# Kernel tuning notes

Measured on AMD Instinct MI355X. Metric: run time of the kernel, lower is better.

Reference implementation:

```python
import jax, jax.numpy as jnp
import numpy as np

E = 512      # embedding_size
H = 8        # heads
FF = 4 * E   # ffn hidden
EPS = 1e-5


def layer_norm(x, gamma, beta):
    mu = jnp.mean(x, axis=-1, keepdims=True)
    var = jnp.mean((x - mu) ** 2, axis=-1, keepdims=True)
    return (x - mu) * jax.lax.rsqrt(var + EPS) * gamma + beta


def setup_inputs() -> dict:
    key = jax.random.key(0)
    ks = jax.random.split(key, 12)
    N, L = 4, 2048
    s = E ** -0.5
    return {
        "x": jax.random.normal(ks[0], (N, L, E), jnp.float32),
        "wq": jax.random.normal(ks[1], (E, E), jnp.float32) * s,
        "wk": jax.random.normal(ks[2], (E, E), jnp.float32) * s,
        "wv": jax.random.normal(ks[3], (E, E), jnp.float32) * s,
        "wo": jax.random.normal(ks[4], (E, E), jnp.float32) * s,
        "bo": jnp.zeros((E,), jnp.float32),
        "g1": jnp.ones((E,), jnp.float32),
        "b1": jnp.zeros((E,), jnp.float32),
        "g2": jnp.ones((E,), jnp.float32),
        "b2": jnp.zeros((E,), jnp.float32),
        "w1": jax.random.normal(ks[5], (E, FF), jnp.float32) * s,
        "bf1": jnp.zeros((FF,), jnp.float32),
        "w2": jax.random.normal(ks[6], (FF, E), jnp.float32) * (FF ** -0.5),
        "bf2": jnp.zeros((E,), jnp.float32),
    }


def reference(x, wq, wk, wv, wo, bo, g1, b1, g2, b2, w1, bf1, w2, bf2):
    N, L, _ = x.shape
    skip = x
    h = layer_norm(x, g1, b1)
    # attention (weights stored as [in, out])
    q = (h @ wq).reshape(N, L, H, E // H)
    k = (h @ wk).reshape(N, L, H, E // H)
    v = (h @ wv).reshape(N, L, H, E // H)
    # NOTE: source scales by embedding_size**-0.5 (not head_dim)
    scores = jnp.einsum('nqhd,nkhd->nhqk', q, k) * (E ** -0.5)
    attn = jax.nn.softmax(scores, axis=-1)
    out = jnp.einsum('nhql,nlhd->nqhd', attn, v).reshape(N, L, E)
    x = out @ wo + bo + skip
    skip = x
    h = layer_norm(x, g2, b2)  # dropout is identity in eval
    h = jax.nn.silu(h @ w1 + bf1) @ w2 + bf2
    return h + skip
```

## Files before the change

kernel.cpp:

```cpp
#include <hip/hip_runtime.h>
#include <hip/hip_bf16.h>

typedef __bf16 bf16;
typedef __attribute__((ext_vector_type(2))) __bf16 bf16x2;
typedef __attribute__((ext_vector_type(8))) __bf16 bf16x8;
typedef __attribute__((ext_vector_type(4))) float f32x4;
typedef __attribute__((ext_vector_type(16))) float f32x16;

#define MFMA16(a, b, c) __builtin_amdgcn_mfma_f32_16x16x32_bf16((a), (b), (c), 0, 0, 0)
#define MFMA32(a, b, c) __builtin_amdgcn_mfma_f32_32x32x16_bf16((a), (b), (c), 0, 0, 0)


__device__ __forceinline__ void load_lds16(const bf16* g, bf16* l) {
    __builtin_amdgcn_global_load_lds(
        (const __attribute__((address_space(1))) void*)g,
        (__attribute__((address_space(3))) void*)l, 16, 0, 0);
}

__device__ __forceinline__ float fexp2(float x) { return __builtin_amdgcn_exp2f(x); }

__global__ void cvt_all(const float* __restrict__ wq, const float* __restrict__ wk,
                        const float* __restrict__ wv, const float* __restrict__ wo,
                        const float* __restrict__ w1, const float* __restrict__ w2,
                        bf16* __restrict__ wqkv_t, bf16* __restrict__ wo_t,
                        bf16* __restrict__ w1_t, bf16* __restrict__ w2_t) {
    __shared__ float t[64][65];
    const int b = blockIdx.x;
    const float* src; bf16* dst;
    int sstride, dstride, r0, c0, dr0;
    if (b < 192) {
        int bx = b % 24, by = b / 24;
        int j0 = bx * 64;
        src = (j0 < 512) ? wq : (j0 < 1024) ? wk : wv;
        sstride = 512; r0 = by * 64; c0 = j0 & 511;
        dst = wqkv_t; dstride = 512; dr0 = j0;
    } else if (b < 256) {
        int tt = b - 192; int bx = tt % 8, by = tt / 8;
        src = wo; sstride = 512; r0 = by * 64; c0 = bx * 64;
        dst = wo_t; dstride = 512; dr0 = c0;
    } else if (b < 512) {
        int tt = b - 256; int bx = tt % 32, by = tt / 32;
        src = w1; sstride = 2048; r0 = by * 64; c0 = bx * 64;
        dst = w1_t; dstride = 512; dr0 = c0;
    } else {
        int tt = b - 512; int bx = tt % 8, by = tt / 8;
        src = w2; sstride = 512; r0 = by * 64; c0 = bx * 64;
        dst = w2_t; dstride = 2048; dr0 = c0;
    }
    #pragma unroll
    for (int p = 0; p < 16; p++) {
        int lin = threadIdx.x + p * 256;
        int rr = lin >> 6, cc = lin & 63;
        t[rr][cc] = src[(size_t)(r0 + rr) * sstride + c0 + cc];
    }
    __syncthreads();
    #pragma unroll
    for (int p = 0; p < 16; p++) {
        int lin = threadIdx.x + p * 256;
        int cc = lin >> 6, rr = lin & 63;
        dst[(size_t)(dr0 + cc) * dstride + r0 + rr] = (bf16)t[rr][cc];
    }
}

__global__ void ln_kernel(const float* __restrict__ x, const float* __restrict__ g,
                          const float* __restrict__ b, bf16* __restrict__ out) {
    int row = blockIdx.x * 4 + (threadIdx.x >> 6);
    int lane = threadIdx.x & 63;
    const float4* xr = (const float4*)(x + (size_t)row * 512);
    float4 v0 = xr[lane];
    float4 v1 = xr[lane + 64];
    float s  = v0.x + v0.y + v0.z + v0.w + v1.x + v1.y + v1.z + v1.w;
    float sq = v0.x*v0.x + v0.y*v0.y + v0.z*v0.z + v0.w*v0.w
             + v1.x*v1.x + v1.y*v1.y + v1.z*v1.z + v1.w*v1.w;
    #pragma unroll
    for (int d = 1; d < 64; d <<= 1) { s += __shfl_xor(s, d); sq += __shfl_xor(sq, d); }
    float mean = s * (1.f / 512.f);
    float var  = sq * (1.f / 512.f) - mean * mean;
    float rs   = rsqrtf(var + 1e-5f);
    const float4* gv = (const float4*)g;
    const float4* bv = (const float4*)b;
    float4 ga = gv[lane], gb = gv[lane + 64];
    float4 ba = bv[lane], bb = bv[lane + 64];
    bf16* orow = out + (size_t)row * 512;
    int c0 = lane * 4;
    orow[c0 + 0]   = (bf16)((v0.x - mean) * rs * ga.x + ba.x);
    orow[c0 + 1]   = (bf16)((v0.y - mean) * rs * ga.y + ba.y);
    orow[c0 + 2]   = (bf16)((v0.z - mean) * rs * ga.z + ba.z);
    orow[c0 + 3]   = (bf16)((v0.w - mean) * rs * ga.w + ba.w);
    orow[c0 + 256] = (bf16)((v1.x - mean) * rs * gb.x + bb.x);
    orow[c0 + 257] = (bf16)((v1.y - mean) * rs * gb.y + bb.y);
    orow[c0 + 258] = (bf16)((v1.z - mean) * rs * gb.z + bb.z);
    orow[c0 + 259] = (bf16)((v1.w - mean) * rs * gb.w + bb.w);
}

template<int KD, int ND, int EPI>
__global__ __launch_bounds__(256, 3) void gemm_k(
        const bf16* __restrict__ A, const bf16* __restrict__ Bt,
        const float* __restrict__ bias, void* __restrict__ outp) {
    __shared__ bf16 As[128 * 64];
    __shared__ bf16 Bs[128 * 64];
    const int bm = blockIdx.x, bn = blockIdx.y;
    const int tid = threadIdx.x;
    const int w = tid >> 6, lane = tid & 63;
    const int wm = (w >> 1) * 64, wn = (w & 1) * 64;
    const int lr = lane & 15, lq = lane >> 4, lr7 = lane & 7;
    const int srow = lane >> 3, gslot = lane & 7;
    f32x4 acc[4][4] = {};
    const bf16* Ab = A + (size_t)bm * 128 * KD;
    const bf16* Bb = Bt + (size_t)bn * 128 * KD;
    const int gcol = (gslot ^ srow) * 8;
    for (int k0 = 0; k0 < KD; k0 += 64) {
        __syncthreads();
        #pragma unroll
        for (int s = 0; s < 4; s++) {
            int rbase = w * 32 + s * 8;
            int row = rbase + srow;
            load_lds16(&Ab[(size_t)row * KD + k0 + gcol], &As[rbase * 64]);
            load_lds16(&Bb[(size_t)row * KD + k0 + gcol], &Bs[rbase * 64]);
        }
        __syncthreads();
        #pragma unroll
        for (int ks = 0; ks < 2; ks++) {
            bf16x8 af[4], bfr[4];
            #pragma unroll
            for (int mi = 0; mi < 4; mi++) {
                int row = wm + mi * 16 + lr;
                af[mi] = *(const bf16x8*)&As[row * 64 + (((ks * 4 + lq) ^ lr7) << 3)];
            }
            #pragma unroll
            for (int ni = 0; ni < 4; ni++) {
                int row = wn + ni * 16 + lr;
                bfr[ni] = *(const bf16x8*)&Bs[row * 64 + (((ks * 4 + lq) ^ lr7) << 3)];
            }
            #pragma unroll
            for (int mi = 0; mi < 4; mi++)
                #pragma unroll
                for (int ni = 0; ni < 4; ni++)
                    acc[mi][ni] = MFMA16(af[mi], bfr[ni], acc[mi][ni]);
        }
    }
    #pragma unroll
    for (int mi = 0; mi < 4; mi++)
        #pragma unroll
        for (int ni = 0; ni < 4; ni++)
            #pragma unroll
            for (int r = 0; r < 4; r++) {
                int row = bm * 128 + wm + mi * 16 + lq * 4 + r;
                int col = bn * 128 + wn + ni * 16 + lr;
                float v = acc[mi][ni][r];
                size_t off = (size_t)row * ND + col;
                if constexpr (EPI == 0) {
                    ((bf16*)outp)[off] = (bf16)v;
                } else {
                    v += bias[col];
                    v = v / (1.f + __expf(-v));
                    ((bf16*)outp)[off] = (bf16)v;
                }
            }
}

template<int KD>
__global__ __launch_bounds__(256, 4) void gemm64(
        const bf16* __restrict__ A, const bf16* __restrict__ Bt,
        const float* __restrict__ bias, const float* __restrict__ resid,
        float* __restrict__ outp) {
    __shared__ bf16 As[64 * 64];
    __shared__ bf16 Bs[64 * 64];
    const int bm = blockIdx.x, bn = blockIdx.y;
    const int tid = threadIdx.x;
    const int w = tid >> 6, lane = tid & 63;
    const int wm = (w >> 1) * 32, wn = (w & 1) * 32;
    const int lr = lane & 15, lq = lane >> 4, lr7 = lane & 7;
    const int srow = lane >> 3, gslot = lane & 7;
    f32x4 acc[2][2] = {};
    const bf16* Ab = A + (size_t)bm * 64 * KD;
    const bf16* Bb = Bt + (size_t)bn * 64 * KD;
    const int gcol = (gslot ^ srow) * 8;
    for (int k0 = 0; k0 < KD; k0 += 64) {
        __syncthreads();
        #pragma unroll
        for (int s = 0; s < 2; s++) {
            int rbase = w * 16 + s * 8;
            int row = rbase + srow;
            load_lds16(&Ab[(size_t)row * KD + k0 + gcol], &As[rbase * 64]);
            load_lds16(&Bb[(size_t)row * KD + k0 + gcol], &Bs[rbase * 64]);
        }
        __syncthreads();
        #pragma unroll
        for (int ks = 0; ks < 2; ks++) {
            bf16x8 af[2], bfr[2];
            #pragma unroll
            for (int mi = 0; mi < 2; mi++) {
                int row = wm + mi * 16 + lr;
                af[mi] = *(const bf16x8*)&As[row * 64 + (((ks * 4 + lq) ^ lr7) << 3)];
            }
            #pragma unroll
            for (int ni = 0; ni < 2; ni++) {
                int row = wn + ni * 16 + lr;
                bfr[ni] = *(const bf16x8*)&Bs[row * 64 + (((ks * 4 + lq) ^ lr7) << 3)];
            }
            #pragma unroll
            for (int mi = 0; mi < 2; mi++)
                #pragma unroll
                for (int ni = 0; ni < 2; ni++)
                    acc[mi][ni] = MFMA16(af[mi], bfr[ni], acc[mi][ni]);
        }
    }
    #pragma unroll
    for (int mi = 0; mi < 2; mi++)
        #pragma unroll
        for (int ni = 0; ni < 2; ni++)
            #pragma unroll
            for (int r = 0; r < 4; r++) {
                int row = bm * 64 + wm + mi * 16 + lq * 4 + r;
                int col = bn * 64 + wn + ni * 16 + lr;
                size_t off = (size_t)row * 512 + col;
                outp[off] = acc[mi][ni][r] + bias[col] + resid[off];
            }
}

__global__ void pack_kv(const bf16* __restrict__ qkvb, bf16* __restrict__ Kfrag,
                        bf16* __restrict__ Vfrag) {
    __shared__ bf16 t[64 * 72];
    const int nh = blockIdx.x & 31, lt = blockIdx.x >> 5;
    const int n = nh >> 3, h = nh & 7;
    const int tid = threadIdx.x;
    #pragma unroll
    for (int p = 0; p < 2; p++) {
        int cid = tid + p * 256;
        int key = lt * 64 + (cid >> 3);
        int dc = cid & 7;
        bf16x8 kv = *(const bf16x8*)&qkvb[(size_t)(n * 2048 + key) * 1536
                                          + 512 + h * 64 + dc * 8];
        int kb = key >> 5, l5 = key & 31;
        int c = dc >> 1, g = dc & 1;
        *(bf16x8*)&Kfrag[(size_t)(((nh * 64 + kb) * 4 + c) * 64 + g * 32 + l5) * 8] = kv;
    }
    #pragma unroll
    for (int p = 0; p < 2; p++) {
        int lin = tid + p * 256;
        int rr = lin >> 3, cc = lin & 7;
        bf16x8 v = *(const bf16x8*)&qkvb[(size_t)(n * 2048 + lt * 64 + rr) * 1536
                                         + 1024 + h * 64 + cc * 8];
        *(bf16x8*)&t[rr * 72 + (cc ^ (rr & 7)) * 8] = v;
    }
    __syncthreads();
    #pragma unroll
    for (int p = 0; p < 2; p++) {
        int lin = tid + p * 256;
        int dd = lin & 63, llc = lin >> 6 | (p << 2);
        bf16x8 o;
        #pragma unroll
        for (int j = 0; j < 8; j++) {
            int ll = llc * 8 + j;
            o[j] = t[ll * 72 + (((dd >> 3) ^ (ll & 7)) * 8) + (dd & 7)];
        }
        int token0 = lt * 64 + llc * 8;
        int kb = token0 >> 5;
        int tl5 = token0 & 31;
        int r = ((tl5 >> 4) << 1) | (dd >> 5);
        int lane = ((token0 >> 3) & 1) * 32 + (dd & 31);
        *(bf16x8*)&Vfrag[(size_t)(((nh * 64 + kb) * 4 + r) * 64 + lane) * 8] = o;
    }
}

__global__ __launch_bounds__(512, 4) void attn_kernel(const bf16* __restrict__ qkv,
                                                      const bf16* __restrict__ Kfrag,
                                                      const bf16* __restrict__ Vfrag,
                                                      bf16* __restrict__ aout) {
    __shared__ float accbuf[4][32][64];
    __shared__ float psumbuf[4][32];
    __shared__ bf16 Ot[4][32 * 72];
    const int b = blockIdx.x;
    const int nh = b & 31;
    const int qt = b >> 5;
    const int n = nh >> 3, h = nh & 7;
    const int tid = threadIdx.x, w = tid >> 6, lane = tid & 63;
    const int qsub = w & 3, ks = w >> 2;
    const int lq5 = lane & 31, g = lane >> 5;
    const float cf = 0.04419417382415922f * 1.4426950408889634f;

    const bf16* Qp = qkv + (size_t)(n * 2048 + qt * 128 + qsub * 32 + lq5) * 1536
                     + h * 64 + g * 8;
    bf16x8 qf[4];
    #pragma unroll
    for (int c = 0; c < 4; c++) {
        bf16x8 raw = *(const bf16x8*)(Qp + c * 16);
        #pragma unroll
        for (int j = 0; j < 8; j++) qf[c][j] = (bf16)((float)raw[j] * cf);
    }

    f32x16 acc0 = {0}, acc1 = {0};
    float psum = 0.f;

    const bf16* Kb = Kfrag + (size_t)((nh * 64 + ks * 32) * 4) * 512 + lane * 8;
    const bf16* Vb = Vfrag + (size_t)((nh * 64 + ks * 32) * 4) * 512 + lane * 8;

    bf16x8 kfn[4];
    kfn[0] = *(const bf16x8*)(Kb);
    kfn[1] = *(const bf16x8*)(Kb + 512);
    kfn[2] = *(const bf16x8*)(Kb + 1024);
    kfn[3] = *(const bf16x8*)(Kb + 1536);

    #pragma unroll 2
    for (int t = 0; t < 32; t++) {
        const bf16* Vc = Vb + t * 2048;
        bf16x8 v00 = *(const bf16x8*)(Vc);
        bf16x8 v01 = *(const bf16x8*)(Vc + 512);
        bf16x8 v10 = *(const bf16x8*)(Vc + 1024);
        bf16x8 v11 = *(const bf16x8*)(Vc + 1536);

        f32x16 st = {0};
        st = MFMA32(kfn[0], qf[0], st);
        st = MFMA32(kfn[1], qf[1], st);
        st = MFMA32(kfn[2], qf[2], st);
        st = MFMA32(kfn[3], qf[3], st);

        if (t < 31) {
            const bf16* Kt = Kb + (t + 1) * 2048;
            kfn[0] = *(const bf16x8*)(Kt);
            kfn[1] = *(const bf16x8*)(Kt + 512);
            kfn[2] = *(const bf16x8*)(Kt + 1024);
            kfn[3] = *(const bf16x8*)(Kt + 1536);
        }

        #pragma unroll
        for (int h16 = 0; h16 < 2; h16++) {
            uint32_t pk[4];
            #pragma unroll
            for (int i = 0; i < 4; i++) {
                float p0 = fexp2(fminf(st[8 * h16 + 2 * i], 60.f));
                float p1 = fexp2(fminf(st[8 * h16 + 2 * i + 1], 60.f));
                psum += p0 + p1;
                union { uint32_t u; bf16x2 hh; } cvu;
                cvu.hh = bf16x2{(bf16)p0, (bf16)p1};
                pk[i] = cvu.u;
            }
            uint32_t s0 = g ? pk[0] : pk[2];
            uint32_t s1 = g ? pk[1] : pk[3];
            uint32_t r0 = (uint32_t)__shfl_xor((int)s0, 32);
            uint32_t r1 = (uint32_t)__shfl_xor((int)s1, 32);
            union { uint4 u; bf16x8 v; } pf;
            pf.u = g == 0 ? uint4{pk[0], pk[1], r0, r1}
                          : uint4{r0, r1, pk[2], pk[3]};
            if (h16 == 0) {
                acc0 = MFMA32(v00, pf.v, acc0);
                acc1 = MFMA32(v01, pf.v, acc1);
            } else {
                acc0 = MFMA32(v10, pf.v, acc0);
                acc1 = MFMA32(v11, pf.v, acc1);
            }
        }
    }

    float tot = psum + __shfl_xor(psum, 32);

    if (ks == 1) {
        #pragma unroll
        for (int r = 0; r < 16; r++) {
            accbuf[qsub][r][lane]      = acc0[r];
            accbuf[qsub][16 + r][lane] = acc1[r];
        }
        if (g == 0) psumbuf[qsub][lq5] = tot;
    }
    __syncthreads();
    if (ks == 0) {
        float inv = 1.f / (tot + psumbuf[qsub][lq5]);
        bf16* ot = Ot[qsub];
        #pragma unroll
        for (int r = 0; r < 16; r++) {
            float a0 = acc0[r] + accbuf[qsub][r][lane];
            float a1 = acc1[r] + accbuf[qsub][16 + r][lane];
            int d0 = (r & 3) + 8 * (r >> 2) + 4 * g;
            ot[lq5 * 72 + d0]      = (bf16)(a0 * inv);
            ot[lq5 * 72 + d0 + 32] = (bf16)(a1 * inv);
        }
        __builtin_amdgcn_s_waitcnt(0);
        #pragma unroll
        for (int i = 0; i < 4; i++) {
            int tq = i * 8 + (lane >> 3);
            bf16x8 ov = *(const bf16x8*)&ot[tq * 72 + (lane & 7) * 8];
            *(bf16x8*)&aout[(size_t)(n * 2048 + qt * 128 + qsub * 32 + tq) * 512
                            + h * 64 + (lane & 7) * 8] = ov;
        }
    }
}

extern "C" void kernel_launch(void* const* d_in, const int* in_sizes, int n_in,
                              void* d_out, int out_size, void* d_ws, size_t ws_size,
                              hipStream_t stream) {
    (void)in_sizes; (void)n_in; (void)out_size; (void)ws_size;
    const float* x   = (const float*)d_in[0];
    const float* wq  = (const float*)d_in[1];
    const float* wk  = (const float*)d_in[2];
    const float* wv  = (const float*)d_in[3];
    const float* wo  = (const float*)d_in[4];
    const float* bo  = (const float*)d_in[5];
    const float* g1  = (const float*)d_in[6];
    const float* b1  = (const float*)d_in[7];
    const float* g2  = (const float*)d_in[8];
    const float* b2  = (const float*)d_in[9];
    const float* w1  = (const float*)d_in[10];
    const float* bf1 = (const float*)d_in[11];
    const float* w2  = (const float*)d_in[12];
    const float* bf2 = (const float*)d_in[13];
    float* out = (float*)d_out;

    char* p = (char*)d_ws;
    bf16*  h1     = (bf16*)p;  p += (size_t)8192 * 512 * 2;
    bf16*  qkvb   = (bf16*)p;  p += (size_t)8192 * 1536 * 2;
    bf16*  aout   = (bf16*)p;  p += (size_t)8192 * 512 * 2;
    float* x2     = (float*)p; p += (size_t)8192 * 512 * 4;
    bf16*  ff1    = (bf16*)p;  p += (size_t)8192 * 2048 * 2;
    bf16*  wqkv_t = (bf16*)p;  p += (size_t)1536 * 512 * 2;
    bf16*  wo_t   = (bf16*)p;  p += (size_t)512 * 512 * 2;
    bf16*  w1_t   = (bf16*)p;  p += (size_t)2048 * 512 * 2;
    bf16*  w2_t   = (bf16*)p;  p += (size_t)512 * 2048 * 2;
    bf16*  Kfrag  = (bf16*)ff1;
    bf16*  Vfrag  = Kfrag + (size_t)8192 * 512;

    cvt_all<<<768, 256, 0, stream>>>(wq, wk, wv, wo, w1, w2, wqkv_t, wo_t, w1_t, w2_t);

    ln_kernel<<<2048, 256, 0, stream>>>(x, g1, b1, h1);
    gemm_k<512, 1536, 0><<<dim3(64, 12), 256, 0, stream>>>(h1, wqkv_t, nullptr, qkvb);
    pack_kv<<<1024, 256, 0, stream>>>(qkvb, Kfrag, Vfrag);
    attn_kernel<<<512, 512, 0, stream>>>(qkvb, Kfrag, Vfrag, aout);
    gemm64<512><<<dim3(128, 8), 256, 0, stream>>>(aout, wo_t, bo, x, x2);
    ln_kernel<<<2048, 256, 0, stream>>>(x2, g2, b2, h1);
    gemm_k<512, 2048, 2><<<dim3(64, 16), 256, 0, stream>>>(h1, w1_t, bf1, ff1);
    gemm64<2048><<<dim3(128, 8), 256, 0, stream>>>(ff1, w2_t, bf2, x2, out);
}
```

Measured before the change: 243.7 us.

## Fuse LN1 into weight conversion, scatter K/V in QKV epilogue, retile output GEMMs

Merges the first layernorm into the weight-conversion launch and drops the separate pack_kv kernel by having the QKV GEMM scatter K and V directly into fragment layouts while writing Q to a compact buffer. The 64x64 gemm64 kernels for the Wo and W2 projections are replaced with the 128x128 gemm_k using a new residual-add epilogue. The clamp before exp2 in attention is also removed. These cut launches and a round trip through qkvb, at the cost of scattered 2-byte stores in the QKV epilogue and only 256 blocks for the N=512 GEMMs. Removing the clamp risks overflow if scores are large.

```diff
diff --git a/kernel.cpp b/kernel.cpp
--- a/kernel.cpp
+++ b/kernel.cpp
@@ -19,13 +19,45 @@
 
 __device__ __forceinline__ float fexp2(float x) { return __builtin_amdgcn_exp2f(x); }
 
-__global__ void cvt_all(const float* __restrict__ wq, const float* __restrict__ wk,
-                        const float* __restrict__ wv, const float* __restrict__ wo,
-                        const float* __restrict__ w1, const float* __restrict__ w2,
-                        bf16* __restrict__ wqkv_t, bf16* __restrict__ wo_t,
-                        bf16* __restrict__ w1_t, bf16* __restrict__ w2_t) {
+__global__ void front_kernel(const float* __restrict__ x, const float* __restrict__ g1,
+                             const float* __restrict__ b1, bf16* __restrict__ h1,
+                             const float* __restrict__ wq, const float* __restrict__ wk,
+                             const float* __restrict__ wv, const float* __restrict__ wo,
+                             const float* __restrict__ w1, const float* __restrict__ w2,
+                             bf16* __restrict__ wqkv_t, bf16* __restrict__ wo_t,
+                             bf16* __restrict__ w1_t, bf16* __restrict__ w2_t) {
     __shared__ float t[64][65];
-    const int b = blockIdx.x;
+    if (blockIdx.x < 2048) {
+        int row = blockIdx.x * 4 + (threadIdx.x >> 6);
+        int lane = threadIdx.x & 63;
+        const float4* xr = (const float4*)(x + (size_t)row * 512);
+        float4 v0 = xr[lane];
+        float4 v1 = xr[lane + 64];
+        float s  = v0.x + v0.y + v0.z + v0.w + v1.x + v1.y + v1.z + v1.w;
+        float sq = v0.x*v0.x + v0.y*v0.y + v0.z*v0.z + v0.w*v0.w
+                 + v1.x*v1.x + v1.y*v1.y + v1.z*v1.z + v1.w*v1.w;
+        #pragma unroll
+        for (int d = 1; d < 64; d <<= 1) { s += __shfl_xor(s, d); sq += __shfl_xor(sq, d); }
+        float mean = s * (1.f / 512.f);
+        float var  = sq * (1.f / 512.f) - mean * mean;
+        float rs   = rsqrtf(var + 1e-5f);
+        const float4* gv = (const float4*)g1;
+        const float4* bv = (const float4*)b1;
+        float4 ga = gv[lane], gb = gv[lane + 64];
+        float4 ba = bv[lane], bb = bv[lane + 64];
+        bf16* orow = h1 + (size_t)row * 512;
+        int c0 = lane * 4;
+        orow[c0 + 0]   = (bf16)((v0.x - mean) * rs * ga.x + ba.x);
+        orow[c0 + 1]   = (bf16)((v0.y - mean) * rs * ga.y + ba.y);
+        orow[c0 + 2]   = (bf16)((v0.z - mean) * rs * ga.z + ba.z);
+        orow[c0 + 3]   = (bf16)((v0.w - mean) * rs * ga.w + ba.w);
+        orow[c0 + 256] = (bf16)((v1.x - mean) * rs * gb.x + bb.x);
+        orow[c0 + 257] = (bf16)((v1.y - mean) * rs * gb.y + bb.y);
+        orow[c0 + 258] = (bf16)((v1.z - mean) * rs * gb.z + bb.z);
+        orow[c0 + 259] = (bf16)((v1.w - mean) * rs * gb.w + bb.w);
+        return;
+    }
+    const int b = blockIdx.x - 2048;
     const float* src; bf16* dst;
     int sstride, dstride, r0, c0, dr0;
     if (b < 192) {
@@ -96,7 +128,8 @@
 template<int KD, int ND, int EPI>
 __global__ __launch_bounds__(256, 3) void gemm_k(
         const bf16* __restrict__ A, const bf16* __restrict__ Bt,
-        const float* __restrict__ bias, void* __restrict__ outp) {
+        const float* __restrict__ bias, const float* __restrict__ resid,
+        void* __restrict__ outp) {
     __shared__ bf16 As[128 * 64];
     __shared__ bf16 Bs[128 * 64];
     const int bm = blockIdx.x, bn = blockIdx.y;
@@ -151,6 +184,8 @@
                 size_t off = (size_t)row * ND + col;
                 if constexpr (EPI == 0) {
                     ((bf16*)outp)[off] = (bf16)v;
+                } else if constexpr (EPI == 1) {
+                    ((float*)outp)[off] = v + bias[col] + resid[off];
                 } else {
                     v += bias[col];
                     v = v / (1.f + __expf(-v));
@@ -159,112 +194,80 @@
             }
 }
 
-template<int KD>
-__global__ __launch_bounds__(256, 4) void gemm64(
+__global__ __launch_bounds__(256, 3) void gemm_qkv(
         const bf16* __restrict__ A, const bf16* __restrict__ Bt,
-        const float* __restrict__ bias, const float* __restrict__ resid,
-        float* __restrict__ outp) {
-    __shared__ bf16 As[64 * 64];
-    __shared__ bf16 Bs[64 * 64];
+        bf16* __restrict__ Qb, bf16* __restrict__ Kfrag, bf16* __restrict__ Vfrag) {
+    __shared__ bf16 As[128 * 64];
+    __shared__ bf16 Bs[128 * 64];
     const int bm = blockIdx.x, bn = blockIdx.y;
     const int tid = threadIdx.x;
     const int w = tid >> 6, lane = tid & 63;
-    const int wm = (w >> 1) * 32, wn = (w & 1) * 32;
+    const int wm = (w >> 1) * 64, wn = (w & 1) * 64;
     const int lr = lane & 15, lq = lane >> 4, lr7 = lane & 7;
     const int srow = lane >> 3, gslot = lane & 7;
-    f32x4 acc[2][2] = {};
-    const bf16* Ab = A + (size_t)bm * 64 * KD;
-    const bf16* Bb = Bt + (size_t)bn * 64 * KD;
+    f32x4 acc[4][4] = {};
+    const bf16* Ab = A + (size_t)bm * 128 * 512;
+    const bf16* Bb = Bt + (size_t)bn * 128 * 512;
     const int gcol = (gslot ^ srow) * 8;
-    for (int k0 = 0; k0 < KD; k0 += 64) {
+    for (int k0 = 0; k0 < 512; k0 += 64) {
         __syncthreads();
         #pragma unroll
-        for (int s = 0; s < 2; s++) {
-            int rbase = w * 16 + s * 8;
+        for (int s = 0; s < 4; s++) {
+            int rbase = w * 32 + s * 8;
             int row = rbase + srow;
-            load_lds16(&Ab[(size_t)row * KD + k0 + gcol], &As[rbase * 64]);
-            load_lds16(&Bb[(size_t)row * KD + k0 + gcol], &Bs[rbase * 64]);
+            load_lds16(&Ab[(size_t)row * 512 + k0 + gcol], &As[rbase * 64]);
+            load_lds16(&Bb[(size_t)row * 512 + k0 + gcol], &Bs[rbase * 64]);
         }
         __syncthreads();
         #pragma unroll
         for (int ks = 0; ks < 2; ks++) {
-            bf16x8 af[2], bfr[2];
-            #pragma unroll
-            for (int mi = 0; mi < 2; mi++) {
+            bf16x8 af[4], bfr[4];
+            #pragma unroll
+            for (int mi = 0; mi < 4; mi++) {
                 int row = wm + mi * 16 + lr;
                 af[mi] = *(const bf16x8*)&As[row * 64 + (((ks * 4 + lq) ^ lr7) << 3)];
             }
             #pragma unroll
-            for (int ni = 0; ni < 2; ni++) {
+            for (int ni = 0; ni < 4; ni++) {
                 int row = wn + ni * 16 + lr;
                 bfr[ni] = *(const bf16x8*)&Bs[row * 64 + (((ks * 4 + lq) ^ lr7) << 3)];
             }
             #pragma unroll
-            for (int mi = 0; mi < 2; mi++)
+            for (int mi = 0; mi < 4; mi++)
                 #pragma unroll
-                for (int ni = 0; ni < 2; ni++)
+                for (int ni = 0; ni < 4; ni++)
                     acc[mi][ni] = MFMA16(af[mi], bfr[ni], acc[mi][ni]);
         }
     }
     #pragma unroll
-    for (int mi = 0; mi < 2; mi++)
-        #pragma unroll
-        for (int ni = 0; ni < 2; ni++)
+    for (int mi = 0; mi < 4; mi++)
+        #pragma unroll
+        for (int ni = 0; ni < 4; ni++)
             #pragma unroll
             for (int r = 0; r < 4; r++) {
-                int row = bm * 64 + wm + mi * 16 + lq * 4 + r;
-                int col = bn * 64 + wn + ni * 16 + lr;
-                size_t off = (size_t)row * 512 + col;
-                outp[off] = acc[mi][ni][r] + bias[col] + resid[off];
-            }
-}
-
-__global__ void pack_kv(const bf16* __restrict__ qkvb, bf16* __restrict__ Kfrag,
-                        bf16* __restrict__ Vfrag) {
-    __shared__ bf16 t[64 * 72];
-    const int nh = blockIdx.x & 31, lt = blockIdx.x >> 5;
-    const int n = nh >> 3, h = nh & 7;
-    const int tid = threadIdx.x;
-    #pragma unroll
-    for (int p = 0; p < 2; p++) {
-        int cid = tid + p * 256;
-        int key = lt * 64 + (cid >> 3);
-        int dc = cid & 7;
-        bf16x8 kv = *(const bf16x8*)&qkvb[(size_t)(n * 2048 + key) * 1536
-                                          + 512 + h * 64 + dc * 8];
-        int kb = key >> 5, l5 = key & 31;
-        int c = dc >> 1, g = dc & 1;
-        *(bf16x8*)&Kfrag[(size_t)(((nh * 64 + kb) * 4 + c) * 64 + g * 32 + l5) * 8] = kv;
-    }
-    #pragma unroll
-    for (int p = 0; p < 2; p++) {
-        int lin = tid + p * 256;
-        int rr = lin >> 3, cc = lin & 7;
-        bf16x8 v = *(const bf16x8*)&qkvb[(size_t)(n * 2048 + lt * 64 + rr) * 1536
-                                         + 1024 + h * 64 + cc * 8];
-        *(bf16x8*)&t[rr * 72 + (cc ^ (rr & 7)) * 8] = v;
-    }
-    __syncthreads();
-    #pragma unroll
-    for (int p = 0; p < 2; p++) {
-        int lin = tid + p * 256;
-        int dd = lin & 63, llc = lin >> 6 | (p << 2);
-        bf16x8 o;
-        #pragma unroll
-        for (int j = 0; j < 8; j++) {
-            int ll = llc * 8 + j;
-            o[j] = t[ll * 72 + (((dd >> 3) ^ (ll & 7)) * 8) + (dd & 7)];
-        }
-        int token0 = lt * 64 + llc * 8;
-        int kb = token0 >> 5;
-        int tl5 = token0 & 31;
-        int r = ((tl5 >> 4) << 1) | (dd >> 5);
-        int lane = ((token0 >> 3) & 1) * 32 + (dd & 31);
-        *(bf16x8*)&Vfrag[(size_t)(((nh * 64 + kb) * 4 + r) * 64 + lane) * 8] = o;
-    }
-}
-
-__global__ __launch_bounds__(512, 4) void attn_kernel(const bf16* __restrict__ qkv,
+                int row = bm * 128 + wm + mi * 16 + lq * 4 + r;
+                int col = bn * 128 + wn + ni * 16 + lr;
+                bf16 v = (bf16)acc[mi][ni][r];
+                if (col < 512) {
+                    Qb[(size_t)row * 512 + col] = v;
+                } else if (col < 1024) {
+                    int h = (col - 512) >> 6, d = (col - 512) & 63;
+                    int n = row >> 11, key = row & 2047, nh = n * 8 + h;
+                    int kb = key >> 5, l5 = key & 31;
+                    int c = d >> 4, g2 = (d >> 3) & 1, j = d & 7;
+                    Kfrag[(size_t)(((nh * 64 + kb) * 4 + c) * 64 + g2 * 32 + l5) * 8 + j] = v;
+                } else {
+                    int h = (col - 1024) >> 6, d = (col - 1024) & 63;
+                    int n = row >> 11, tok = row & 2047, nh = n * 8 + h;
+                    int kb = tok >> 5, j = tok & 7;
+                    int rr2 = (((tok >> 4) & 1) << 1) | (d >> 5);
+                    int ln2 = ((tok >> 3) & 1) * 32 + (d & 31);
+                    Vfrag[(size_t)(((nh * 64 + kb) * 4 + rr2) * 64 + ln2) * 8 + j] = v;
+                }
+            }
+}
+
+__global__ __launch_bounds__(512, 4) void attn_kernel(const bf16* __restrict__ Qb,
                                                       const bf16* __restrict__ Kfrag,
                                                       const bf16* __restrict__ Vfrag,
                                                       bf16* __restrict__ aout) {
@@ -280,7 +283,7 @@
     const int lq5 = lane & 31, g = lane >> 5;
     const float cf = 0.04419417382415922f * 1.4426950408889634f;
 
-    const bf16* Qp = qkv + (size_t)(n * 2048 + qt * 128 + qsub * 32 + lq5) * 1536
+    const bf16* Qp = Qb + (size_t)(n * 2048 + qt * 128 + qsub * 32 + lq5) * 512
                      + h * 64 + g * 8;
     bf16x8 qf[4];
     #pragma unroll
@@ -329,8 +332,8 @@
             uint32_t pk[4];
             #pragma unroll
             for (int i = 0; i < 4; i++) {
-                float p0 = fexp2(fminf(st[8 * h16 + 2 * i], 60.f));
-                float p1 = fexp2(fminf(st[8 * h16 + 2 * i + 1], 60.f));
+                float p0 = fexp2(st[8 * h16 + 2 * i]);
+                float p1 = fexp2(st[8 * h16 + 2 * i + 1]);
                 psum += p0 + p1;
                 union { uint32_t u; bf16x2 hh; } cvu;
                 cvu.hh = bf16x2{(bf16)p0, (bf16)p1};
@@ -408,7 +411,7 @@
 
     char* p = (char*)d_ws;
     bf16*  h1     = (bf16*)p;  p += (size_t)8192 * 512 * 2;
-    bf16*  qkvb   = (bf16*)p;  p += (size_t)8192 * 1536 * 2;
+    bf16*  Qb     = (bf16*)p;  p += (size_t)8192 * 512 * 2;
     bf16*  aout   = (bf16*)p;  p += (size_t)8192 * 512 * 2;
     float* x2     = (float*)p; p += (size_t)8192 * 512 * 4;
     bf16*  ff1    = (bf16*)p;  p += (size_t)8192 * 2048 * 2;
@@ -419,14 +422,12 @@
     bf16*  Kfrag  = (bf16*)ff1;
     bf16*  Vfrag  = Kfrag + (size_t)8192 * 512;
 
-    cvt_all<<<768, 256, 0, stream>>>(wq, wk, wv, wo, w1, w2, wqkv_t, wo_t, w1_t, w2_t);
-
-    ln_kernel<<<2048, 256, 0, stream>>>(x, g1, b1, h1);
-    gemm_k<512, 1536, 0><<<dim3(64, 12), 256, 0, stream>>>(h1, wqkv_t, nullptr, qkvb);
-    pack_kv<<<1024, 256, 0, stream>>>(qkvb, Kfrag, Vfrag);
-    attn_kernel<<<512, 512, 0, stream>>>(qkvb, Kfrag, Vfrag, aout);
-    gemm64<512><<<dim3(128, 8), 256, 0, stream>>>(aout, wo_t, bo, x, x2);
+    front_kernel<<<2816, 256, 0, stream>>>(x, g1, b1, h1, wq, wk, wv, wo, w1, w2,
+                                           wqkv_t, wo_t, w1_t, w2_t);
+    gemm_qkv<<<dim3(64, 12), 256, 0, stream>>>(h1, wqkv_t, Qb, Kfrag, Vfrag);
+    attn_kernel<<<512, 512, 0, stream>>>(Qb, Kfrag, Vfrag, aout);
+    gemm_k<512, 512, 1><<<dim3(64, 4), 256, 0, stream>>>(aout, wo_t, bo, x, x2);
     ln_kernel<<<2048, 256, 0, stream>>>(x2, g2, b2, h1);
-    gemm_k<512, 2048, 2><<<dim3(64, 16), 256, 0, stream>>>(h1, w1_t, bf1, ff1);
-    gemm64<2048><<<dim3(128, 8), 256, 0, stream>>>(ff1, w2_t, bf2, x2, out);
-}
+    gemm_k<512, 2048, 2><<<dim3(64, 16), 256, 0, stream>>>(h1, w1_t, bf1, nullptr, ff1);
+    gemm_k<2048, 512, 1><<<dim3(64, 4), 256, 0, stream>>>(ff1, w2_t, bf2, x2, out);
+}
```

After: 248.6 us. +2.0%, slower.
